# Kernel tuning notes

Hardware: AMD Instinct MI355X
Metric: run time of the kernel (lower is better)

Reference implementation:

```python
import jax, jax.numpy as jnp
import numpy as np

B, L, D, H = 2, 256, 512, 8
DV = D // H
INF = 1e12

def _xavier(key, shape, fan_in, fan_out):
    a = float(np.sqrt(6.0 / (fan_in + fan_out)))
    return jax.random.uniform(key, shape, minval=-a, maxval=a, dtype=jnp.float32)

def setup_inputs() -> dict:
    key = jax.random.key(0)
    ks = jax.random.split(key, 9)
    inp = jax.random.normal(ks[0], (B, L, D), dtype=jnp.float32)
    relation_inp = jax.random.normal(ks[1], (B, L, L, D), dtype=jnp.float32)
    mask = jax.random.randint(ks[2], (B, L, L), 0, 2).astype(bool)
    adj_mask = jax.random.randint(ks[3], (B, H, L, L), 0, 2).astype(jnp.float32)
    W_value = _xavier(ks[4], (D, H * DV), D, H * DV)
    W_relation = _xavier(ks[5], (D, H * DV), D, H * DV)
    # weight vectors have torch shape (1,1,1,H,DV); xavier fans over last two dims
    w_src = _xavier(ks[6], (H, DV), H, DV)
    w_tgt = _xavier(ks[7], (H, DV), H, DV)
    w_rel = _xavier(ks[8], (H, DV), H, DV)
    return {"inp": inp, "relation_inp": relation_inp, "mask": mask,
            "adj_mask": adj_mask, "W_value": W_value, "W_relation": W_relation,
            "w_src": w_src, "w_tgt": w_tgt, "w_rel": w_rel}

def reference(inp, relation_inp, mask, adj_mask, W_value, W_relation, w_src, w_tgt, w_rel):
    b, l, d = inp.shape
    h, dv = w_src.shape
    # value: (B,H,L,DV)
    value = (inp @ W_value).reshape(b, l, h, dv).transpose(0, 2, 1, 3)
    # relation: (B,L,L,H,DV)
    relation = (relation_inp @ W_relation).reshape(b, l, l, h, dv)
    # scores[b,h,i,j] = w_src.v_j + w_tgt.v_i + w_rel.rel[b,i,j,h]
    s_src = jnp.einsum('bhjd,hd->bhj', value, w_src)[:, :, None, :]
    s_tgt = jnp.einsum('bhid,hd->bhi', value, w_tgt)[:, :, :, None]
    s_rel = jnp.einsum('bijhd,hd->bhij', relation, w_rel)
    scores = s_src + s_tgt + s_rel
    scores = jnp.where(scores >= 0, scores, 0.2 * scores)  # LeakyReLU(0.2)
    m = mask[:, None]  # (B,1,L,L)
    adj_zero = adj_mask == 0
    scores = jnp.where(m, -INF, scores)
    scores = jnp.where(adj_zero, -INF, scores)
    attn = jax.nn.softmax(scores, axis=-1)
    # normalized: divide by edge weight (zeros -> weight INF -> 1/INF)
    inv = jnp.where(adj_zero, 1.0 / INF, 1.0 / jnp.where(adj_zero, 1.0, adj_mask))
    attn = attn * inv
    attn = attn / jnp.maximum(jnp.sum(jnp.abs(attn), axis=-1, keepdims=True), 1e-12)
    attn = jnp.where(m, 0.0, attn)
    attn = jnp.where(adj_zero, 0.0, attn)
    out = jnp.einsum('bhij,bhjd->bhid', attn, value)
    out = out.transpose(0, 2, 1, 3).reshape(b, l, d)  # concat heads
    return out + inp
```

## Files before the change

kernel.cpp:

```cpp
#include <hip/hip_runtime.h>

#define B_ 2
#define L_ 256
#define D_ 512
#define H_ 8
#define DV_ 64
#define NEGINF 1e12f

#define WS_VALUE 0
#define WS_WR    262144
#define WS_SSRC  266240
#define WS_STGT  270336

#define GLOAD_LDS16(g, l)                                                     \
    __builtin_amdgcn_global_load_lds(                                         \
        (const __attribute__((address_space(1))) void*)(g),                   \
        (__attribute__((address_space(3))) void*)(l), 16, 0, 0)

__global__ __launch_bounds__(256) void k_wr(const float* __restrict__ Wrel,
                                            const float* __restrict__ wrel,
                                            float* __restrict__ WR) {
    int flat = blockIdx.x * 256 + threadIdx.x;
    int k = flat >> 3, h = flat & 7;
    const float* a = Wrel + k * 512 + h * 64;
    const float* b = wrel + h * 64;
    float s = 0.f;
#pragma unroll
    for (int d = 0; d < 64; d += 4) {
        float4 x = *(const float4*)(a + d);
        float4 y = *(const float4*)(b + d);
        s += x.x * y.x + x.y * y.y + x.z * y.z + x.w * y.w;
    }
    WR[k * 8 + h] = s;
}

__global__ __launch_bounds__(256) void k_value(const float* __restrict__ inp,
                                               const float* __restrict__ Wv,
                                               float* __restrict__ value) {
    int blk = blockIdx.x;
    int ct  = blk & 1;
    int rt  = blk >> 1;
    int n   = ct * 256 + threadIdx.x;
    int r0  = rt * 4;
    const float* i0 = inp + (size_t)(r0 + 0) * 512;
    const float* i1 = inp + (size_t)(r0 + 1) * 512;
    const float* i2 = inp + (size_t)(r0 + 2) * 512;
    const float* i3 = inp + (size_t)(r0 + 3) * 512;
    float a0 = 0.f, a1 = 0.f, a2 = 0.f, a3 = 0.f;
#pragma unroll 16
    for (int k = 0; k < 512; ++k) {
        float w = Wv[(size_t)k * 512 + n];
        a0 = fmaf(i0[k], w, a0);
        a1 = fmaf(i1[k], w, a1);
        a2 = fmaf(i2[k], w, a2);
        a3 = fmaf(i3[k], w, a3);
    }
    int h = n >> 6, dv = n & 63;
    float acc[4] = {a0, a1, a2, a3};
#pragma unroll
    for (int r = 0; r < 4; ++r) {
        int row = r0 + r;
        int b = row >> 8, l = row & 255;
        value[(((size_t)(b * 8 + h)) * 256 + l) * 64 + dv] = acc[r];
    }
}

__global__ __launch_bounds__(256) void k_src_tgt(const float* __restrict__ value,
                                                 const float* __restrict__ wsrc,
                                                 const float* __restrict__ wtgt,
                                                 float* __restrict__ s_src,
                                                 float* __restrict__ s_tgt) {
    int flat = blockIdx.x * 256 + threadIdx.x;
    int h = (flat >> 8) & 7;
    const float* v  = value + (size_t)flat * 64;
    const float* ws = wsrc + h * 64;
    const float* wt = wtgt + h * 64;
    float ss = 0.f, st = 0.f;
#pragma unroll
    for (int d = 0; d < 64; d += 4) {
        float4 x = *(const float4*)(v + d);
        float4 s4 = *(const float4*)(ws + d);
        float4 t4 = *(const float4*)(wt + d);
        ss += x.x * s4.x + x.y * s4.y + x.z * s4.z + x.w * s4.w;
        st += x.x * t4.x + x.y * t4.y + x.z * t4.z + x.w * t4.w;
    }
    s_src[flat] = ss;
    s_tgt[flat] = st;
}

__global__ __launch_bounds__(256) void k_main(const float* __restrict__ rel,
                                              const int*   __restrict__ mask,
                                              const float* __restrict__ adj,
                                              const float* __restrict__ inp,
                                              const float* __restrict__ value,
                                              const float* __restrict__ WR,
                                              const float* __restrict__ s_src,
                                              const float* __restrict__ s_tgt,
                                              float* __restrict__ out) {
    __shared__ float lds[16384];
    int bi   = blockIdx.x;
    int b    = bi >> 8;
    int i    = bi & 255;
    int tid  = threadIdx.x;
    int w    = tid >> 6;
    int lane = tid & 63;

    const float* relbase = rel + (size_t)bi * 256 * 512;

    const float* gsrc[8];
    {
#pragma unroll
        for (int s = 0; s < 8; ++s) {
            int f = w * 512 + s * 64 + lane;
            int r = f >> 3, c = f & 7;
            int cp = c ^ (r & 7);
            gsrc[s] = relbase + (size_t)r * 512 + cp * 4;
        }
    }

#define STAGE(bufofs, k0)                                                      \
    {                                                                          \
        _Pragma("unroll")                                                      \
        for (int s = 0; s < 8; ++s)                                            \
            GLOAD_LDS16(gsrc[s] + (k0), &lds[(bufofs) + w * 2048 + s * 256]);  \
    }

    float acc[8];
#pragma unroll
    for (int h = 0; h < 8; ++h) acc[h] = 0.f;

    int tswz = tid & 7;

    STAGE(0, 0);
    for (int kt = 0; kt < 16; ++kt) {
        int cur = (kt & 1) * 8192;
        if (kt < 15) {
            int nxt = ((kt + 1) & 1) * 8192;
            STAGE(nxt, (kt + 1) * 32);
            asm volatile("s_waitcnt vmcnt(8)" ::: "memory");
        } else {
            asm volatile("s_waitcnt vmcnt(0)" ::: "memory");
        }
        const float* myrow = &lds[cur + tid * 32];
        const float* wrt   = WR + kt * 32 * 8;
#pragma unroll
        for (int q = 0; q < 8; ++q) {
            float4 x = *(const float4*)&myrow[(q ^ tswz) << 2];
#pragma unroll
            for (int h = 0; h < 8; ++h) {
                acc[h] = fmaf(x.x, wrt[(q * 4 + 0) * 8 + h],
                         fmaf(x.y, wrt[(q * 4 + 1) * 8 + h],
                         fmaf(x.z, wrt[(q * 4 + 2) * 8 + h],
                         fmaf(x.w, wrt[(q * 4 + 3) * 8 + h], acc[h]))));
            }
        }
    }

    __syncthreads();
    float* srel_s = lds;
    float* attn_s = lds + 2048;
#pragma unroll
    for (int h = 0; h < 8; ++h) srel_s[h * 256 + tid] = acc[h];
    __syncthreads();

    {
        int h  = tid >> 5;
        int ln = tid & 31;
        float stgt = s_tgt[(size_t)(b * 8 + h) * 256 + i];
        const float* ssrc   = s_src + (size_t)(b * 8 + h) * 256;
        const float* adjrow = adj + ((size_t)(b * 8 + h) * 256 + i) * 256;
        const int*   mrow   = mask + (size_t)bi * 256;

        float sc[8], av[8];
        int mb = 0;
        float rowmax = -3.0e38f;
#pragma unroll
        for (int t = 0; t < 8; ++t) {
            int j = ln + 32 * t;
            float a = adjrow[j];
            av[t] = a;
            int m = mrow[j];
            float s = ssrc[j] + stgt + srel_s[h * 256 + j];
            s = (s >= 0.f) ? s : 0.2f * s;
            if (m != 0) { s = -NEGINF; mb |= (1 << t); }
            if (a == 0.f) s = -NEGINF;
            sc[t] = s;
            rowmax = fmaxf(rowmax, s);
        }
#pragma unroll
        for (int off = 16; off >= 1; off >>= 1)
            rowmax = fmaxf(rowmax, __shfl_xor(rowmax, off));

        float rowsum = 0.f;
#pragma unroll
        for (int t = 0; t < 8; ++t) {
            sc[t] = expf(sc[t] - rowmax);
            rowsum += sc[t];
        }
#pragma unroll
        for (int off = 16; off >= 1; off >>= 1)
            rowsum += __shfl_xor(rowsum, off);

        float sumabs = 0.f;
#pragma unroll
        for (int t = 0; t < 8; ++t) {
            float p = sc[t] / rowsum;
            float invv = (av[t] == 0.f) ? 1e-12f : (1.0f / av[t]);
            p *= invv;
            sc[t] = p;
            sumabs += fabsf(p);
        }
#pragma unroll
        for (int off = 16; off >= 1; off >>= 1)
            sumabs += __shfl_xor(sumabs, off);

        float rdn = 1.0f / fmaxf(sumabs, 1e-12f);
#pragma unroll
        for (int t = 0; t < 8; ++t) {
            float p = sc[t] * rdn;
            if (mb & (1 << t)) p = 0.f;
            if (av[t] == 0.f) p = 0.f;
            attn_s[h * 256 + ln + 32 * t] = p;
        }
    }
    __syncthreads();

    {
        int h  = tid >> 5;
        int d0 = (tid & 31) * 2;
        const float* vbase = value + ((size_t)(b * 8 + h) * 256) * 64 + d0;
        const float* arow  = attn_s + h * 256;
        float ax = 0.f, ay = 0.f;
#pragma unroll 4
        for (int j = 0; j < 256; ++j) {
            float a = arow[j];
            float2 v2 = *(const float2*)(vbase + (size_t)j * 64);
            ax = fmaf(a, v2.x, ax);
            ay = fmaf(a, v2.y, ay);
        }
        size_t o = (size_t)bi * 512 + h * 64 + d0;
        out[o]     = inp[o] + ax;
        out[o + 1] = inp[o + 1] + ay;
    }
}

extern "C" void kernel_launch(void* const* d_in, const int* in_sizes, int n_in,
                              void* d_out, int out_size, void* d_ws, size_t ws_size,
                              hipStream_t stream) {
    const float* inp      = (const float*)d_in[0];
    const float* rel      = (const float*)d_in[1];
    const int*   mask     = (const int*)  d_in[2];
    const float* adj      = (const float*)d_in[3];
    const float* W_value  = (const float*)d_in[4];
    const float* W_rel    = (const float*)d_in[5];
    const float* w_src    = (const float*)d_in[6];
    const float* w_tgt    = (const float*)d_in[7];
    const float* w_rel    = (const float*)d_in[8];
    float* out = (float*)d_out;

    float* ws    = (float*)d_ws;
    float* value = ws + WS_VALUE;
    float* WR    = ws + WS_WR;
    float* s_src = ws + WS_SSRC;
    float* s_tgt = ws + WS_STGT;

    k_wr<<<16, 256, 0, stream>>>(W_rel, w_rel, WR);
    k_value<<<256, 256, 0, stream>>>(inp, W_value, value);
    k_src_tgt<<<16, 256, 0, stream>>>(value, w_src, w_tgt, s_src, s_tgt);
    k_main<<<B_ * L_, 256, 0, stream>>>(rel, mask, adj, inp, value, WR,
                                        s_src, s_tgt, out);
}
```

Measured before the change: 123.6 us.

## Fuse src/tgt score reduction into value GEMM and halve k_main LDS staging tile

Drops the separate k_src_tgt kernel. k_value now computes the w_src/w_tgt dot products with a wavefront shuffle reduction over the 64 dv lanes, which removes one launch and a re-read of value. k_main's double-buffered relation staging shrinks from 32 to 16 columns per stage, with 32 iterations instead of 16 and an adjusted swizzle. This halves LDS use so more blocks can be resident per CU, at the cost of shallower prefetch per stage and more waits. The unroll of the final attention-value loop also goes from 4 to 8.

```diff
diff --git a/kernel.cpp b/kernel.cpp
--- a/kernel.cpp
+++ b/kernel.cpp
@@ -36,7 +36,11 @@
 
 __global__ __launch_bounds__(256) void k_value(const float* __restrict__ inp,
                                                const float* __restrict__ Wv,
-                                               float* __restrict__ value) {
+                                               const float* __restrict__ wsrc,
+                                               const float* __restrict__ wtgt,
+                                               float* __restrict__ value,
+                                               float* __restrict__ s_src,
+                                               float* __restrict__ s_tgt) {
     int blk = blockIdx.x;
     int ct  = blk & 1;
     int rt  = blk >> 1;
@@ -57,35 +61,25 @@
     }
     int h = n >> 6, dv = n & 63;
     float acc[4] = {a0, a1, a2, a3};
+    float wsv = wsrc[h * 64 + dv];
+    float wtv = wtgt[h * 64 + dv];
 #pragma unroll
     for (int r = 0; r < 4; ++r) {
         int row = r0 + r;
         int b = row >> 8, l = row & 255;
         value[(((size_t)(b * 8 + h)) * 256 + l) * 64 + dv] = acc[r];
-    }
-}
-
-__global__ __launch_bounds__(256) void k_src_tgt(const float* __restrict__ value,
-                                                 const float* __restrict__ wsrc,
-                                                 const float* __restrict__ wtgt,
-                                                 float* __restrict__ s_src,
-                                                 float* __restrict__ s_tgt) {
-    int flat = blockIdx.x * 256 + threadIdx.x;
-    int h = (flat >> 8) & 7;
-    const float* v  = value + (size_t)flat * 64;
-    const float* ws = wsrc + h * 64;
-    const float* wt = wtgt + h * 64;
-    float ss = 0.f, st = 0.f;
-#pragma unroll
-    for (int d = 0; d < 64; d += 4) {
-        float4 x = *(const float4*)(v + d);
-        float4 s4 = *(const float4*)(ws + d);
-        float4 t4 = *(const float4*)(wt + d);
-        ss += x.x * s4.x + x.y * s4.y + x.z * s4.z + x.w * s4.w;
-        st += x.x * t4.x + x.y * t4.y + x.z * t4.z + x.w * t4.w;
-    }
-    s_src[flat] = ss;
-    s_tgt[flat] = st;
+        float ss = acc[r] * wsv;
+        float st = acc[r] * wtv;
+#pragma unroll
+        for (int off = 32; off >= 1; off >>= 1) {
+            ss += __shfl_xor(ss, off);
+            st += __shfl_xor(st, off);
+        }
+        if (dv == 0) {
+            s_src[(size_t)(b * 8 + h) * 256 + l] = ss;
+            s_tgt[(size_t)(b * 8 + h) * 256 + l] = st;
+        }
+    }
 }
 
 __global__ __launch_bounds__(256) void k_main(const float* __restrict__ rel,
@@ -97,7 +91,7 @@
                                               const float* __restrict__ s_src,
                                               const float* __restrict__ s_tgt,
                                               float* __restrict__ out) {
-    __shared__ float lds[16384];
+    __shared__ float lds[8192];
     int bi   = blockIdx.x;
     int b    = bi >> 8;
     int i    = bi & 255;
@@ -107,13 +101,14 @@
 
     const float* relbase = rel + (size_t)bi * 256 * 512;
 
-    const float* gsrc[8];
+    const float* gsrc[4];
     {
 #pragma unroll
-        for (int s = 0; s < 8; ++s) {
-            int f = w * 512 + s * 64 + lane;
-            int r = f >> 3, c = f & 7;
-            int cp = c ^ (r & 7);
+        for (int s = 0; s < 4; ++s) {
+            int f = s * 64 + lane;
+            int rl = f >> 2, c = f & 3;
+            int r = w * 64 + rl;
+            int cp = c ^ (r & 3);
             gsrc[s] = relbase + (size_t)r * 512 + cp * 4;
         }
     }
@@ -121,30 +116,30 @@
 #define STAGE(bufofs, k0)                                                      \
     {                                                                          \
         _Pragma("unroll")                                                      \
-        for (int s = 0; s < 8; ++s)                                            \
-            GLOAD_LDS16(gsrc[s] + (k0), &lds[(bufofs) + w * 2048 + s * 256]);  \
+        for (int s = 0; s < 4; ++s)                                            \
+            GLOAD_LDS16(gsrc[s] + (k0), &lds[(bufofs) + w * 1024 + s * 256]);  \
     }
 
     float acc[8];
 #pragma unroll
     for (int h = 0; h < 8; ++h) acc[h] = 0.f;
 
-    int tswz = tid & 7;
+    int tswz = tid & 3;
 
     STAGE(0, 0);
-    for (int kt = 0; kt < 16; ++kt) {
-        int cur = (kt & 1) * 8192;
-        if (kt < 15) {
-            int nxt = ((kt + 1) & 1) * 8192;
-            STAGE(nxt, (kt + 1) * 32);
-            asm volatile("s_waitcnt vmcnt(8)" ::: "memory");
+    for (int kt = 0; kt < 32; ++kt) {
+        int cur = (kt & 1) * 4096;
+        if (kt < 31) {
+            int nxt = ((kt + 1) & 1) * 4096;
+            STAGE(nxt, (kt + 1) * 16);
+            asm volatile("s_waitcnt vmcnt(4)" ::: "memory");
         } else {
             asm volatile("s_waitcnt vmcnt(0)" ::: "memory");
         }
-        const float* myrow = &lds[cur + tid * 32];
-        const float* wrt   = WR + kt * 32 * 8;
-#pragma unroll
-        for (int q = 0; q < 8; ++q) {
+        const float* myrow = &lds[cur + tid * 16];
+        const float* wrt   = WR + kt * 16 * 8;
+#pragma unroll
+        for (int q = 0; q < 4; ++q) {
             float4 x = *(const float4*)&myrow[(q ^ tswz) << 2];
 #pragma unroll
             for (int h = 0; h < 8; ++h) {
@@ -231,7 +226,7 @@
         const float* vbase = value + ((size_t)(b * 8 + h) * 256) * 64 + d0;
         const float* arow  = attn_s + h * 256;
         float ax = 0.f, ay = 0.f;
-#pragma unroll 4
+#pragma unroll 8
         for (int j = 0; j < 256; ++j) {
             float a = arow[j];
             float2 v2 = *(const float2*)(vbase + (size_t)j * 64);
@@ -265,8 +260,8 @@
     float* s_tgt = ws + WS_STGT;
 
     k_wr<<<16, 256, 0, stream>>>(W_rel, w_rel, WR);
-    k_value<<<256, 256, 0, stream>>>(inp, W_value, value);
-    k_src_tgt<<<16, 256, 0, stream>>>(value, w_src, w_tgt, s_src, s_tgt);
+    k_value<<<256, 256, 0, stream>>>(inp, W_value, w_src, w_tgt,
+                                     value, s_src, s_tgt);
     k_main<<<B_ * L_, 256, 0, stream>>>(rel, mask, adj, inp, value, WR,
                                         s_src, s_tgt, out);
 }
```

Result: faster. 118.4 us (-4.2%).
